# Kernel optimization log

Measured on AMD Instinct MI355X. Metric: run time of the kernel, lower is better.

## Reference

```python
import jax, jax.numpy as jnp
import numpy as np
import math

B, S, E = 2, 2048, 1024
H, HD = 16, 64  # num_heads, head_size


def setup_inputs() -> dict:
    key = jax.random.key(0)
    ks = jax.random.split(key, 9)
    sc = 1.0 / math.sqrt(HD)
    return {
        "x": jax.random.normal(ks[0], (B, S, E), dtype=jnp.float32),
        "Wq_w": jax.random.normal(ks[1], (HD, HD), dtype=jnp.float32) * sc,
        "Wq_b": jax.random.normal(ks[2], (HD,), dtype=jnp.float32) * 0.02,
        "Wk_w": jax.random.normal(ks[3], (HD, HD), dtype=jnp.float32) * sc,
        "Wk_b": jax.random.normal(ks[4], (HD,), dtype=jnp.float32) * 0.02,
        "Wv_w": jax.random.normal(ks[5], (HD, HD), dtype=jnp.float32) * sc,
        "Wv_b": jax.random.normal(ks[6], (HD,), dtype=jnp.float32) * 0.02,
        "proj_w": jax.random.normal(ks[7], (E, E), dtype=jnp.float32) * (1.0 / math.sqrt(E)),
        "proj_b": jax.random.normal(ks[8], (E,), dtype=jnp.float32) * 0.02,
    }


def reference(x, Wq_w, Wq_b, Wk_w, Wk_b, Wv_w, Wv_b, proj_w, proj_b):
    b, s, _ = x.shape
    xh = x.reshape(b, s, H, HD)  # split heads; QKV linears act per-head (shared weights)
    # torch Linear: y = x @ W.T + b
    q = jnp.einsum('bshd,ed->bhse', xh, Wq_w) + Wq_b  # [B,H,S,HD]
    k = jnp.einsum('bshd,ed->bhse', xh, Wk_w) + Wk_b
    v = jnp.einsum('bshd,ed->bhse', xh, Wv_w) + Wv_b
    scores = jnp.einsum('bhqd,bhkd->bhqk', q, k) / math.sqrt(HD)
    causal = jnp.tril(jnp.ones((s, s), dtype=bool))
    scores = jnp.where(causal, scores, jnp.float32(-1e20))
    attn = jax.nn.softmax(scores, axis=-1)  # attn_dropout p=0 (eval)
    out = jnp.einsum('bhqk,bhkd->bqhd', attn, v).reshape(b, s, H * HD)
    out = out @ proj_w.T + proj_b  # resid_dropout p=0 (eval)
    return out
```

## Files before the change

kernel.cpp:

```cpp
#include <hip/hip_runtime.h>
#include <hip/hip_bf16.h>

#define B_ 2
#define S_ 2048
#define E_ 1024
#define H_ 16
#define HD_ 64
#define T_ (B_ * S_)

typedef short bf16x8 __attribute__((ext_vector_type(8)));
typedef short bf16x4 __attribute__((ext_vector_type(4)));
typedef float f32x4 __attribute__((ext_vector_type(4)));

__device__ __forceinline__ short f2bf(float f) {
  union { float f; unsigned u; } v;
  v.f = f;
  unsigned r = v.u + 0x7fffu + ((v.u >> 16) & 1u);
  return (short)(r >> 16);
}


__global__ __launch_bounds__(256) void qkv_conv_kernel(
    const float* __restrict__ x,
    const float* __restrict__ wq, const float* __restrict__ bq,
    const float* __restrict__ wk, const float* __restrict__ bk,
    const float* __restrict__ wv, const float* __restrict__ bv,
    short* __restrict__ Q, short* __restrict__ KV,
    const float* __restrict__ pw, short* __restrict__ pwb) {
  const int tid = threadIdx.x;
  if (blockIdx.x >= 512) {
    int i = ((blockIdx.x - 512) * 256 + tid) * 4;
    float4 f = *(const float4*)(pw + i);
    bf16x4 o;
    o[0] = f2bf(f.x); o[1] = f2bf(f.y); o[2] = f2bf(f.z); o[3] = f2bf(f.w);
    *(bf16x4*)(pwb + i) = o;
    return;
  }
  __shared__ short Xs[64][136];
  __shared__ short Ws[192][72];
  __shared__ short Qt[64][68], Kt[64][68], Vt[64][68];

  const int bid = blockIdx.x;
  const int tb = bid >> 3, hg = bid & 7;
  const int s0 = (tb * 64) & (S_ - 1);
  const int kt = s0 >> 6;
  const int bb = (tb * 64) >> 11;
  const int wave = tid >> 6, lane = tid & 63;
  const int lrow = lane & 15, quad = lane >> 4;

#pragma unroll
  for (int i = 0; i < 8; i++) {
    int c = tid + 256 * i;
    int row = c >> 5, col4 = c & 31;
    float4 f = *(const float4*)(x + ((long)(tb * 64 + row)) * E_ + hg * 128 + col4 * 4);
    bf16x4 o;
    o[0] = f2bf(f.x); o[1] = f2bf(f.y); o[2] = f2bf(f.z); o[3] = f2bf(f.w);
    *(bf16x4*)&Xs[row][col4 * 4] = o;
  }
#pragma unroll
  for (int m = 0; m < 3; m++) {
    const float* w = (m == 0) ? wq : (m == 1) ? wk : wv;
#pragma unroll
    for (int i = 0; i < 4; i++) {
      int c = tid + 256 * i;
      int row = m * 64 + (c >> 4), col = (c & 15) * 4;
      float4 f = *(const float4*)(w + (long)c * 4);
      bf16x4 o;
      o[0] = f2bf(f.x); o[1] = f2bf(f.y); o[2] = f2bf(f.z); o[3] = f2bf(f.w);
      *(bf16x4*)&Ws[row][col] = o;
    }
  }
  float bias[12];
#pragma unroll
  for (int nb = 0; nb < 12; nb++) {
    int sel = nb >> 2;
    int e = ((nb & 3) * 16) + lrow;
    bias[nb] = ((sel == 0) ? bq : (sel == 1) ? bk : bv)[e];
  }
  __syncthreads();

  bf16x8 bf0[12], bf1[12];
#pragma unroll
  for (int nb = 0; nb < 12; nb++) {
    bf0[nb] = *(bf16x8*)&Ws[nb * 16 + lrow][quad * 8];
    bf1[nb] = *(bf16x8*)&Ws[nb * 16 + lrow][32 + quad * 8];
  }

  const float QSCALE = 0.125f * 1.44269504089f;
  for (int hl = 0; hl < 2; hl++) {
    const int h = hg * 2 + hl;
    bf16x8 a0 = *(bf16x8*)&Xs[wave * 16 + lrow][hl * 64 + quad * 8];
    bf16x8 a1 = *(bf16x8*)&Xs[wave * 16 + lrow][hl * 64 + 32 + quad * 8];
#pragma unroll
    for (int nb = 0; nb < 12; nb++) {
      f32x4 acc = {0.f, 0.f, 0.f, 0.f};
      acc = __builtin_amdgcn_mfma_f32_16x16x32_bf16(a0, bf0[nb], acc, 0, 0, 0);
      acc = __builtin_amdgcn_mfma_f32_16x16x32_bf16(a1, bf1[nb], acc, 0, 0, 0);
      const int sel = nb >> 2;
      const float scale = (sel == 0) ? QSCALE : 1.0f;
      short (*ct)[68] = (sel == 0) ? Qt : (sel == 1) ? Kt : Vt;
#pragma unroll
      for (int r = 0; r < 4; r++) {
        ct[wave * 16 + quad * 4 + r][(nb & 3) * 16 + lrow] =
            f2bf((acc[r] + bias[nb]) * scale);
      }
    }
    __syncthreads();

    const int bh = bb * H_ + h;
    short* Qg = Q + ((long)bh * S_ + s0) * HD_;
    short* Tg = KV + ((long)(bh * 32 + kt)) * 8192;
#pragma unroll
    for (int i = 0; i < 2; i++) {
      int c = tid + 256 * i;
      int row = c >> 3, col = (c & 7) * 8;
      *(bf16x8*)(Qg + (long)row * HD_ + col) = *(bf16x8*)&Qt[row][col];
    }
#pragma unroll
    for (int u = 0; u < 4; u++) {
      int fid = tid + 256 * u;
      bf16x8 val;
      int lane2 = fid & 63;
      int quad2 = lane2 >> 4, lrow2 = lane2 & 15;
      if (u < 2) {
        int g = fid >> 6;
        int nb = g >> 1, half = g & 1;
        val = *(bf16x8*)&Kt[nb * 16 + lrow2][half * 32 + quad2 * 8];
      } else {
        int g = (fid >> 6) & 7;
        int p2 = g >> 2, db = g & 3;
#pragma unroll
        for (int j = 0; j < 8; j++) {
          int key = (2 * p2 + (j >> 2)) * 16 + quad2 * 4 + (j & 3);
          val[j] = Vt[key][db * 16 + lrow2];
        }
      }
      *(bf16x8*)(Tg + fid * 8) = val;
    }
    __syncthreads();
  }
}

__global__ __launch_bounds__(128) void attn_kernel(
    const short* __restrict__ Q, const short* __restrict__ KV,
    short* __restrict__ O ) {
  const int tid = threadIdx.x;
  const int bid = blockIdx.x;
  const int bh = bid & 31;
  const int g = 31 - (bid >> 5);
  const int b = bh >> 4, h = bh & 15;
  const long qbase = ((long)bh) << 17;

  const int wave = tid >> 6, lane = tid & 63;
  const int lrow = lane & 15, quad = lane >> 4;
  const int r0 = g * 64 + wave * 32;
  const int qgA = r0 + lrow;
  const int qgB = r0 + 16 + lrow;

  const short* qpA = Q + qbase + (long)qgA * HD_;
  const short* qpB = Q + qbase + (long)qgB * HD_;
  bf16x8 qfA0 = *(const bf16x8*)(qpA + quad * 8);
  bf16x8 qfA1 = *(const bf16x8*)(qpA + 32 + quad * 8);
  bf16x8 qfB0 = *(const bf16x8*)(qpB + quad * 8);
  bf16x8 qfB1 = *(const bf16x8*)(qpB + 32 + quad * 8);

  const short* tb = KV + ((long)bh * 32) * 8192 + lane * 8;

  f32x4 OA[4], OB[4];
#pragma unroll
  for (int db = 0; db < 4; db++) {
    OA[db] = f32x4{0.f, 0.f, 0.f, 0.f};
    OB[db] = f32x4{0.f, 0.f, 0.f, 0.f};
  }
  float lsA = 0.f, lsB = 0.f;

  const int nkt = (r0 + 95) >> 6;
  for (int kt = 0; kt < nkt; kt++) {
    const short* tp = tb + (long)kt * 8192;

    bf16x8 kf[8];
#pragma unroll
    for (int g2 = 0; g2 < 8; g2++) kf[g2] = *(const bf16x8*)(tp + g2 * 512);

    f32x4 scA[4], scB[4];
#pragma unroll
    for (int nb = 0; nb < 4; nb++) {
      f32x4 a = {0.f, 0.f, 0.f, 0.f};
      a = __builtin_amdgcn_mfma_f32_16x16x32_bf16(kf[2 * nb], qfA0, a, 0, 0, 0);
      a = __builtin_amdgcn_mfma_f32_16x16x32_bf16(kf[2 * nb + 1], qfA1, a, 0, 0, 0);
      scA[nb] = a;
      f32x4 c = {0.f, 0.f, 0.f, 0.f};
      c = __builtin_amdgcn_mfma_f32_16x16x32_bf16(kf[2 * nb], qfB0, c, 0, 0, 0);
      c = __builtin_amdgcn_mfma_f32_16x16x32_bf16(kf[2 * nb + 1], qfB1, c, 0, 0, 0);
      scB[nb] = c;
    }

    bf16x8 vf[8];
#pragma unroll
    for (int g2 = 0; g2 < 8; g2++) vf[g2] = *(const bf16x8*)(tp + 4096 + g2 * 512);

    if (kt == nkt - 1) {
      const int k0 = kt * 64;
#pragma unroll
      for (int nb = 0; nb < 4; nb++) {
        int kgl = k0 + nb * 16 + quad * 4;
#pragma unroll
        for (int r = 0; r < 4; r++) {
          if (kgl + r > qgA) scA[nb][r] = -1e30f;
          if (kgl + r > qgB) scB[nb][r] = -1e30f;
        }
      }
    }

    bf16x4 pfA[4], pfB[4];
#pragma unroll
    for (int nb = 0; nb < 4; nb++) {
      unsigned ua[4], ub[4];
#pragma unroll
      for (int r = 0; r < 4; r++) {
        float pa = __builtin_amdgcn_exp2f(scA[nb][r]);
        float pb2 = __builtin_amdgcn_exp2f(scB[nb][r]);
        lsA += pa; lsB += pb2;
        ua[r] = __float_as_uint(pa) + 0x8000u;
        ub[r] = __float_as_uint(pb2) + 0x8000u;
      }
      union { unsigned q[2]; bf16x4 v; } pk;
      pk.q[0] = __builtin_amdgcn_perm(ua[1], ua[0], 0x07060302u);
      pk.q[1] = __builtin_amdgcn_perm(ua[3], ua[2], 0x07060302u);
      pfA[nb] = pk.v;
      pk.q[0] = __builtin_amdgcn_perm(ub[1], ub[0], 0x07060302u);
      pk.q[1] = __builtin_amdgcn_perm(ub[3], ub[2], 0x07060302u);
      pfB[nb] = pk.v;
    }

#pragma unroll
    for (int p2 = 0; p2 < 2; p2++) {
#pragma unroll
      for (int db = 0; db < 4; db++) {
        bf16x8 vv = vf[p2 * 4 + db];
        bf16x4 vlo = {vv[0], vv[1], vv[2], vv[3]};
        bf16x4 vhi = {vv[4], vv[5], vv[6], vv[7]};
        OA[db] = __builtin_amdgcn_mfma_f32_16x16x16bf16_1k(vlo, pfA[2 * p2], OA[db], 0, 0, 0);
        OA[db] = __builtin_amdgcn_mfma_f32_16x16x16bf16_1k(vhi, pfA[2 * p2 + 1], OA[db], 0, 0, 0);
        OB[db] = __builtin_amdgcn_mfma_f32_16x16x16bf16_1k(vlo, pfB[2 * p2], OB[db], 0, 0, 0);
        OB[db] = __builtin_amdgcn_mfma_f32_16x16x16bf16_1k(vhi, pfB[2 * p2 + 1], OB[db], 0, 0, 0);
      }
    }
  }

  lsA += __shfl_xor(lsA, 16);
  lsA += __shfl_xor(lsA, 32);
  lsB += __shfl_xor(lsB, 16);
  lsB += __shfl_xor(lsB, 32);
  const float invA = 1.f / lsA, invB = 1.f / lsB;
  short* oA = O + ((long)b * S_ + qgA) * E_ + h * HD_;
  short* oB = O + ((long)b * S_ + qgB) * E_ + h * HD_;
#pragma unroll
  for (int db = 0; db < 4; db++) {
    bf16x4 oa, ob;
#pragma unroll
    for (int r = 0; r < 4; r++) {
      oa[r] = f2bf(OA[db][r] * invA);
      ob[r] = f2bf(OB[db][r] * invB);
    }
    *(bf16x4*)(oA + db * 16 + quad * 4) = oa;
    *(bf16x4*)(oB + db * 16 + quad * 4) = ob;
  }
}

__global__ __launch_bounds__(256) void proj_kernel(
    const short* __restrict__ A, const short* __restrict__ W,
    const float* __restrict__ bias, float* __restrict__ out) {
  __shared__ short As[2][128][40];
  __shared__ short Bs[2][64][40];
  const int tid = threadIdx.x;
  const int bid = blockIdx.x;
  const int m0 = (bid >> 4) * 128;
  const int n0 = (bid & 15) * 64;
  const int wave = tid >> 6, lane = tid & 63;
  const int wm = wave >> 1, wn = wave & 1;
  const int lrow = lane & 15, quad = lane >> 4;

  const int ar = tid >> 1, ac = (tid & 1) * 16;
  const int br = tid >> 2, bc = (tid & 3) * 8;

  bf16x8 a0, a1, b0;
  auto LDR = [&](int k0) {
    const short* ap = A + (long)(m0 + ar) * E_ + k0 + ac;
    a0 = *(const bf16x8*)(ap);
    a1 = *(const bf16x8*)(ap + 8);
    b0 = *(const bf16x8*)(W + (long)(n0 + br) * E_ + k0 + bc);
  };

  f32x4 acc[4][2];
#pragma unroll
  for (int i = 0; i < 4; i++)
#pragma unroll
    for (int j = 0; j < 2; j++) acc[i][j] = f32x4{0.f, 0.f, 0.f, 0.f};

  LDR(0);
  for (int kk = 0; kk < 32; kk++) {
    const int buf = kk & 1;
    *(bf16x8*)&As[buf][ar][ac] = a0;
    *(bf16x8*)&As[buf][ar][ac + 8] = a1;
    *(bf16x8*)&Bs[buf][br][bc] = b0;
    __syncthreads();
    if (kk < 31) LDR((kk + 1) * 32);

    bf16x8 af[4], bfr[2];
#pragma unroll
    for (int i = 0; i < 4; i++)
      af[i] = *(bf16x8*)&As[buf][wm * 64 + i * 16 + lrow][quad * 8];
#pragma unroll
    for (int j = 0; j < 2; j++)
      bfr[j] = *(bf16x8*)&Bs[buf][wn * 32 + j * 16 + lrow][quad * 8];
#pragma unroll
    for (int i = 0; i < 4; i++)
#pragma unroll
      for (int j = 0; j < 2; j++)
        acc[i][j] = __builtin_amdgcn_mfma_f32_16x16x32_bf16(af[i], bfr[j], acc[i][j], 0, 0, 0);
  }

#pragma unroll
  for (int j = 0; j < 2; j++) {
    int col = n0 + wn * 32 + j * 16 + lrow;
    float bv = bias[col];
#pragma unroll
    for (int i = 0; i < 4; i++) {
#pragma unroll
      for (int r = 0; r < 4; r++) {
        int row = m0 + wm * 64 + i * 16 + quad * 4 + r;
        out[(long)row * E_ + col] = acc[i][j][r] + bv;
      }
    }
  }
}

extern "C" void kernel_launch(void* const* d_in, const int* in_sizes, int n_in,
                              void* d_out, int out_size, void* d_ws, size_t ws_size,
                              hipStream_t stream) {
  const float* x  = (const float*)d_in[0];
  const float* wq = (const float*)d_in[1];
  const float* bq = (const float*)d_in[2];
  const float* wk = (const float*)d_in[3];
  const float* bk = (const float*)d_in[4];
  const float* wv = (const float*)d_in[5];
  const float* bv = (const float*)d_in[6];
  const float* pw = (const float*)d_in[7];
  const float* pb = (const float*)d_in[8];
  float* out = (float*)d_out;

  char* ws = (char*)d_ws;
  short* Qb = (short*)(ws);
  short* KVb = (short*)(ws + (size_t)8 * 1024 * 1024);
  short* AO = (short*)(ws + (size_t)24 * 1024 * 1024);
  short* PW = (short*)(ws + (size_t)32 * 1024 * 1024);

  qkv_conv_kernel<<<dim3(512 + 1024), dim3(256), 0, stream>>>(
      x, wq, bq, wk, bk, wv, bv, Qb, KVb, pw, PW);
  attn_kernel<<<dim3(32 * 32), dim3(128), 0, stream>>>(Qb, KVb, AO);
  proj_kernel<<<dim3(32 * 16), dim3(256), 0, stream>>>(AO, PW, pb, out);
}
```

Before: 159.2 us.

## Split attention key tiles across two wave pairs and compute row sums via MFMA

Doubles the attention block to four waves. Each pair of waves handles alternating key tiles for the same 64 query rows, and the partial outputs are combined through shared memory at the end. The softmax denominator is now accumulated with extra MFMAs against a ones vector instead of scalar adds. The bf16 rounding bias on P is also dropped. The aim is more parallelism and shorter per-wave serial loops on causal attention, at the cost of an LDS reduction, a block sync and extra MFMA work for the sums.

New measurement: 149.9 us. -5.8%, faster.

```diff
diff --git a/kernel.cpp b/kernel.cpp
--- a/kernel.cpp
+++ b/kernel.cpp
@@ -141,9 +141,11 @@
   }
 }
 
-__global__ __launch_bounds__(128) void attn_kernel(
+__global__ __launch_bounds__(256, 4) void attn_kernel(
     const short* __restrict__ Q, const short* __restrict__ KV,
     short* __restrict__ O ) {
+  __shared__ float Cmb[2][64][36];
+
   const int tid = threadIdx.x;
   const int bid = blockIdx.x;
   const int bh = bid & 31;
@@ -152,8 +154,10 @@
   const long qbase = ((long)bh) << 17;
 
   const int wave = tid >> 6, lane = tid & 63;
+  const int s = wave & 1;
+  const int c = wave >> 1;
   const int lrow = lane & 15, quad = lane >> 4;
-  const int r0 = g * 64 + wave * 32;
+  const int r0 = g * 64 + s * 32;
   const int qgA = r0 + lrow;
   const int qgB = r0 + 16 + lrow;
 
@@ -172,10 +176,14 @@
     OA[db] = f32x4{0.f, 0.f, 0.f, 0.f};
     OB[db] = f32x4{0.f, 0.f, 0.f, 0.f};
   }
-  float lsA = 0.f, lsB = 0.f;
-
-  const int nkt = (r0 + 95) >> 6;
-  for (int kt = 0; kt < nkt; kt++) {
+  f32x4 OSa = {0.f, 0.f, 0.f, 0.f}, OSb = {0.f, 0.f, 0.f, 0.f};
+  const bf16x4 ones = {(short)0x3F80, (short)0x3F80, (short)0x3F80, (short)0x3F80};
+
+  const int nkt = g + 1;
+  const int nc = (nkt - c + 1) >> 1;
+
+  for (int i = 0; i < nc; i++) {
+    const int kt = c + 2 * i;
     const short* tp = tb + (long)kt * 8192;
 
     bf16x8 kf[8];
@@ -189,10 +197,10 @@
       a = __builtin_amdgcn_mfma_f32_16x16x32_bf16(kf[2 * nb], qfA0, a, 0, 0, 0);
       a = __builtin_amdgcn_mfma_f32_16x16x32_bf16(kf[2 * nb + 1], qfA1, a, 0, 0, 0);
       scA[nb] = a;
-      f32x4 c = {0.f, 0.f, 0.f, 0.f};
-      c = __builtin_amdgcn_mfma_f32_16x16x32_bf16(kf[2 * nb], qfB0, c, 0, 0, 0);
-      c = __builtin_amdgcn_mfma_f32_16x16x32_bf16(kf[2 * nb + 1], qfB1, c, 0, 0, 0);
-      scB[nb] = c;
+      f32x4 cc = {0.f, 0.f, 0.f, 0.f};
+      cc = __builtin_amdgcn_mfma_f32_16x16x32_bf16(kf[2 * nb], qfB0, cc, 0, 0, 0);
+      cc = __builtin_amdgcn_mfma_f32_16x16x32_bf16(kf[2 * nb + 1], qfB1, cc, 0, 0, 0);
+      scB[nb] = cc;
     }
 
     bf16x8 vf[8];
@@ -218,11 +226,8 @@
       unsigned ua[4], ub[4];
 #pragma unroll
       for (int r = 0; r < 4; r++) {
-        float pa = __builtin_amdgcn_exp2f(scA[nb][r]);
-        float pb2 = __builtin_amdgcn_exp2f(scB[nb][r]);
-        lsA += pa; lsB += pb2;
-        ua[r] = __float_as_uint(pa) + 0x8000u;
-        ub[r] = __float_as_uint(pb2) + 0x8000u;
+        ua[r] = __float_as_uint(__builtin_amdgcn_exp2f(scA[nb][r]));
+        ub[r] = __float_as_uint(__builtin_amdgcn_exp2f(scB[nb][r]));
       }
       union { unsigned q[2]; bf16x4 v; } pk;
       pk.q[0] = __builtin_amdgcn_perm(ua[1], ua[0], 0x07060302u);
@@ -245,26 +250,47 @@
         OB[db] = __builtin_amdgcn_mfma_f32_16x16x16bf16_1k(vlo, pfB[2 * p2], OB[db], 0, 0, 0);
         OB[db] = __builtin_amdgcn_mfma_f32_16x16x16bf16_1k(vhi, pfB[2 * p2 + 1], OB[db], 0, 0, 0);
       }
-    }
-  }
-
-  lsA += __shfl_xor(lsA, 16);
-  lsA += __shfl_xor(lsA, 32);
-  lsB += __shfl_xor(lsB, 16);
-  lsB += __shfl_xor(lsB, 32);
-  const float invA = 1.f / lsA, invB = 1.f / lsB;
-  short* oA = O + ((long)b * S_ + qgA) * E_ + h * HD_;
-  short* oB = O + ((long)b * S_ + qgB) * E_ + h * HD_;
-#pragma unroll
-  for (int db = 0; db < 4; db++) {
-    bf16x4 oa, ob;
-#pragma unroll
-    for (int r = 0; r < 4; r++) {
-      oa[r] = f2bf(OA[db][r] * invA);
-      ob[r] = f2bf(OB[db][r] * invB);
-    }
-    *(bf16x4*)(oA + db * 16 + quad * 4) = oa;
-    *(bf16x4*)(oB + db * 16 + quad * 4) = ob;
+      OSa = __builtin_amdgcn_mfma_f32_16x16x16bf16_1k(ones, pfA[2 * p2], OSa, 0, 0, 0);
+      OSa = __builtin_amdgcn_mfma_f32_16x16x16bf16_1k(ones, pfA[2 * p2 + 1], OSa, 0, 0, 0);
+      OSb = __builtin_amdgcn_mfma_f32_16x16x16bf16_1k(ones, pfB[2 * p2], OSb, 0, 0, 0);
+      OSb = __builtin_amdgcn_mfma_f32_16x16x16bf16_1k(ones, pfB[2 * p2 + 1], OSb, 0, 0, 0);
+    }
+  }
+
+  if (c == 1) {
+#pragma unroll
+    for (int db = 0; db < 4; db++) {
+      *(float4*)&Cmb[s][lane][db * 4] =
+          make_float4(OA[db][0], OA[db][1], OA[db][2], OA[db][3]);
+      *(float4*)&Cmb[s][lane][16 + db * 4] =
+          make_float4(OB[db][0], OB[db][1], OB[db][2], OB[db][3]);
+    }
+    Cmb[s][lane][32] = OSa[0];
+    Cmb[s][lane][33] = OSb[0];
+  }
+  __syncthreads();
+  if (c == 0) {
+    float lsA = OSa[0] + Cmb[s][lane][32];
+    float lsB = OSb[0] + Cmb[s][lane][33];
+    const float invA = 1.f / lsA, invB = 1.f / lsB;
+    short* oA = O + ((long)b * S_ + qgA) * E_ + h * HD_;
+    short* oB = O + ((long)b * S_ + qgB) * E_ + h * HD_;
+#pragma unroll
+    for (int db = 0; db < 4; db++) {
+      float4 pa = *(float4*)&Cmb[s][lane][db * 4];
+      float4 pb2 = *(float4*)&Cmb[s][lane][16 + db * 4];
+      bf16x4 oa, ob;
+      oa[0] = f2bf((OA[db][0] + pa.x) * invA);
+      oa[1] = f2bf((OA[db][1] + pa.y) * invA);
+      oa[2] = f2bf((OA[db][2] + pa.z) * invA);
+      oa[3] = f2bf((OA[db][3] + pa.w) * invA);
+      ob[0] = f2bf((OB[db][0] + pb2.x) * invB);
+      ob[1] = f2bf((OB[db][1] + pb2.y) * invB);
+      ob[2] = f2bf((OB[db][2] + pb2.z) * invB);
+      ob[3] = f2bf((OB[db][3] + pb2.w) * invB);
+      *(bf16x4*)(oA + db * 16 + quad * 4) = oa;
+      *(bf16x4*)(oB + db * 16 + quad * 4) = ob;
+    }
   }
 }
 
@@ -358,6 +384,6 @@
 
   qkv_conv_kernel<<<dim3(512 + 1024), dim3(256), 0, stream>>>(
       x, wq, bq, wk, bk, wv, bv, Qb, KVb, pw, PW);
-  attn_kernel<<<dim3(32 * 32), dim3(128), 0, stream>>>(Qb, KVb, AO);
+  attn_kernel<<<dim3(32 * 32), dim3(256), 0, stream>>>(Qb, KVb, AO);
   proj_kernel<<<dim3(32 * 16), dim3(256), 0, stream>>>(AO, PW, pb, out);
 }
```

## Share K/V tiles via double-buffered LDS across four waves in attention

Applied to the files above, without the earlier changes.

The attention kernel now runs 256-thread blocks covering 128 query rows, with four waves sharing K/V tiles staged cooperatively into a double-buffered LDS array, prefetched into registers one tile ahead. Previously each 2-wave block loaded its K/V tiles straight from global memory per wave. The A/B row split is changed so the A rows skip the final fully-masked tile, and block ordering is interleaved heavy/light for load balance. This cuts redundant global loads but adds LDS traffic, a barrier per tile, and fewer blocks, which may reduce occupancy. The bf16 rounding bias (+0x8000) is also dropped, so values are now truncated.

New measurement: 140.3 us. 1.13x faster.

```diff
diff --git a/kernel.cpp b/kernel.cpp
--- a/kernel.cpp
+++ b/kernel.cpp
@@ -141,21 +141,23 @@
   }
 }
 
-__global__ __launch_bounds__(128) void attn_kernel(
+__global__ __launch_bounds__(256, 2) void attn_kernel(
     const short* __restrict__ Q, const short* __restrict__ KV,
     short* __restrict__ O ) {
+  __shared__ short L[2][8192];
+
   const int tid = threadIdx.x;
   const int bid = blockIdx.x;
   const int bh = bid & 31;
-  const int g = 31 - (bid >> 5);
+  const int pr = bid >> 5;
+  const int g = (pr < 8) ? (15 - pr) : (pr - 8);
   const int b = bh >> 4, h = bh & 15;
   const long qbase = ((long)bh) << 17;
 
   const int wave = tid >> 6, lane = tid & 63;
   const int lrow = lane & 15, quad = lane >> 4;
-  const int r0 = g * 64 + wave * 32;
-  const int qgA = r0 + lrow;
-  const int qgB = r0 + 16 + lrow;
+  const int qgA = g * 128 + wave * 16 + lrow;
+  const int qgB = qgA + 64;
 
   const short* qpA = Q + qbase + (long)qgA * HD_;
   const short* qpB = Q + qbase + (long)qgB * HD_;
@@ -164,7 +166,13 @@
   bf16x8 qfB0 = *(const bf16x8*)(qpB + quad * 8);
   bf16x8 qfB1 = *(const bf16x8*)(qpB + 32 + quad * 8);
 
-  const short* tb = KV + ((long)bh * 32) * 8192 + lane * 8;
+  const short* Tg = KV + ((long)bh * 32) * 8192 + tid * 8;
+  bf16x8 reg[4];
+  auto LD = [&](int kt) {
+    const short* p = Tg + (long)kt * 8192;
+#pragma unroll
+    for (int u = 0; u < 4; u++) reg[u] = *(const bf16x8*)(p + u * 2048);
+  };
 
   f32x4 OA[4], OB[4];
 #pragma unroll
@@ -174,63 +182,97 @@
   }
   float lsA = 0.f, lsB = 0.f;
 
-  const int nkt = (r0 + 95) >> 6;
+  const int nkt = 2 * g + 2;
+  LD(0);
   for (int kt = 0; kt < nkt; kt++) {
-    const short* tp = tb + (long)kt * 8192;
+    const int buf = kt & 1;
+#pragma unroll
+    for (int u = 0; u < 4; u++)
+      *(bf16x8*)&L[buf][(tid + 256 * u) * 8] = reg[u];
+    __syncthreads();
+    if (kt + 1 < nkt) LD(kt + 1);
 
     bf16x8 kf[8];
 #pragma unroll
-    for (int g2 = 0; g2 < 8; g2++) kf[g2] = *(const bf16x8*)(tp + g2 * 512);
+    for (int g2 = 0; g2 < 8; g2++)
+      kf[g2] = *(bf16x8*)&L[buf][g2 * 512 + lane * 8];
+
+    const bool doA = (kt < nkt - 1);
 
     f32x4 scA[4], scB[4];
 #pragma unroll
     for (int nb = 0; nb < 4; nb++) {
-      f32x4 a = {0.f, 0.f, 0.f, 0.f};
-      a = __builtin_amdgcn_mfma_f32_16x16x32_bf16(kf[2 * nb], qfA0, a, 0, 0, 0);
-      a = __builtin_amdgcn_mfma_f32_16x16x32_bf16(kf[2 * nb + 1], qfA1, a, 0, 0, 0);
-      scA[nb] = a;
-      f32x4 c = {0.f, 0.f, 0.f, 0.f};
-      c = __builtin_amdgcn_mfma_f32_16x16x32_bf16(kf[2 * nb], qfB0, c, 0, 0, 0);
-      c = __builtin_amdgcn_mfma_f32_16x16x32_bf16(kf[2 * nb + 1], qfB1, c, 0, 0, 0);
-      scB[nb] = c;
+      f32x4 cb = {0.f, 0.f, 0.f, 0.f};
+      cb = __builtin_amdgcn_mfma_f32_16x16x32_bf16(kf[2 * nb], qfB0, cb, 0, 0, 0);
+      cb = __builtin_amdgcn_mfma_f32_16x16x32_bf16(kf[2 * nb + 1], qfB1, cb, 0, 0, 0);
+      scB[nb] = cb;
+    }
+    if (doA) {
+#pragma unroll
+      for (int nb = 0; nb < 4; nb++) {
+        f32x4 ca = {0.f, 0.f, 0.f, 0.f};
+        ca = __builtin_amdgcn_mfma_f32_16x16x32_bf16(kf[2 * nb], qfA0, ca, 0, 0, 0);
+        ca = __builtin_amdgcn_mfma_f32_16x16x32_bf16(kf[2 * nb + 1], qfA1, ca, 0, 0, 0);
+        scA[nb] = ca;
+      }
     }
 
     bf16x8 vf[8];
 #pragma unroll
-    for (int g2 = 0; g2 < 8; g2++) vf[g2] = *(const bf16x8*)(tp + 4096 + g2 * 512);
-
+    for (int g2 = 0; g2 < 8; g2++)
+      vf[g2] = *(bf16x8*)&L[buf][4096 + g2 * 512 + lane * 8];
+
+    if (kt == nkt - 2) {
+      const int k0 = kt * 64;
+#pragma unroll
+      for (int nb = 0; nb < 4; nb++) {
+        int kgl = k0 + nb * 16 + quad * 4;
+#pragma unroll
+        for (int r = 0; r < 4; r++)
+          if (kgl + r > qgA) scA[nb][r] = -1e30f;
+      }
+    }
     if (kt == nkt - 1) {
       const int k0 = kt * 64;
 #pragma unroll
       for (int nb = 0; nb < 4; nb++) {
         int kgl = k0 + nb * 16 + quad * 4;
 #pragma unroll
-        for (int r = 0; r < 4; r++) {
-          if (kgl + r > qgA) scA[nb][r] = -1e30f;
+        for (int r = 0; r < 4; r++)
           if (kgl + r > qgB) scB[nb][r] = -1e30f;
-        }
       }
     }
 
     bf16x4 pfA[4], pfB[4];
 #pragma unroll
     for (int nb = 0; nb < 4; nb++) {
-      unsigned ua[4], ub[4];
+      unsigned ub[4];
 #pragma unroll
       for (int r = 0; r < 4; r++) {
-        float pa = __builtin_amdgcn_exp2f(scA[nb][r]);
-        float pb2 = __builtin_amdgcn_exp2f(scB[nb][r]);
-        lsA += pa; lsB += pb2;
-        ua[r] = __float_as_uint(pa) + 0x8000u;
-        ub[r] = __float_as_uint(pb2) + 0x8000u;
+        float p = __builtin_amdgcn_exp2f(scB[nb][r]);
+        lsB += p;
+        ub[r] = __float_as_uint(p);
       }
       union { unsigned q[2]; bf16x4 v; } pk;
-      pk.q[0] = __builtin_amdgcn_perm(ua[1], ua[0], 0x07060302u);
-      pk.q[1] = __builtin_amdgcn_perm(ua[3], ua[2], 0x07060302u);
-      pfA[nb] = pk.v;
       pk.q[0] = __builtin_amdgcn_perm(ub[1], ub[0], 0x07060302u);
       pk.q[1] = __builtin_amdgcn_perm(ub[3], ub[2], 0x07060302u);
       pfB[nb] = pk.v;
+    }
+    if (doA) {
+#pragma unroll
+      for (int nb = 0; nb < 4; nb++) {
+        unsigned ua[4];
+#pragma unroll
+        for (int r = 0; r < 4; r++) {
+          float p = __builtin_amdgcn_exp2f(scA[nb][r]);
+          lsA += p;
+          ua[r] = __float_as_uint(p);
+        }
+        union { unsigned q[2]; bf16x4 v; } pk;
+        pk.q[0] = __builtin_amdgcn_perm(ua[1], ua[0], 0x07060302u);
+        pk.q[1] = __builtin_amdgcn_perm(ua[3], ua[2], 0x07060302u);
+        pfA[nb] = pk.v;
+      }
     }
 
 #pragma unroll
@@ -240,10 +282,12 @@
         bf16x8 vv = vf[p2 * 4 + db];
         bf16x4 vlo = {vv[0], vv[1], vv[2], vv[3]};
         bf16x4 vhi = {vv[4], vv[5], vv[6], vv[7]};
-        OA[db] = __builtin_amdgcn_mfma_f32_16x16x16bf16_1k(vlo, pfA[2 * p2], OA[db], 0, 0, 0);
-        OA[db] = __builtin_amdgcn_mfma_f32_16x16x16bf16_1k(vhi, pfA[2 * p2 + 1], OA[db], 0, 0, 0);
         OB[db] = __builtin_amdgcn_mfma_f32_16x16x16bf16_1k(vlo, pfB[2 * p2], OB[db], 0, 0, 0);
         OB[db] = __builtin_amdgcn_mfma_f32_16x16x16bf16_1k(vhi, pfB[2 * p2 + 1], OB[db], 0, 0, 0);
+        if (doA) {
+          OA[db] = __builtin_amdgcn_mfma_f32_16x16x16bf16_1k(vlo, pfA[2 * p2], OA[db], 0, 0, 0);
+          OA[db] = __builtin_amdgcn_mfma_f32_16x16x16bf16_1k(vhi, pfA[2 * p2 + 1], OA[db], 0, 0, 0);
+        }
       }
     }
   }
@@ -358,6 +402,6 @@
 
   qkv_conv_kernel<<<dim3(512 + 1024), dim3(256), 0, stream>>>(
       x, wq, bq, wk, bk, wv, bv, Qb, KVb, pw, PW);
-  attn_kernel<<<dim3(32 * 32), dim3(128), 0, stream>>>(Qb, KVb, AO);
+  attn_kernel<<<dim3(16 * 32), dim3(256), 0, stream>>>(Qb, KVb, AO);
   proj_kernel<<<dim3(32 * 16), dim3(256), 0, stream>>>(AO, PW, pb, out);
 }
```
